# Performance work log

Hardware: AMD Instinct MI355X
Metric: run time of the kernel (lower is better)

The kernel has to match this reference:

```python
import jax, jax.numpy as jnp
import numpy as np

N_NODES = 100000


def gcn_conv(x, edge_index, W, b):
    """PyG GCNConv: h = x @ W; out = D^-1/2 (A+I) D^-1/2 h + b."""
    n = x.shape[0]
    src, dst = edge_index[0], edge_index[1]
    loop = jnp.arange(n)
    src = jnp.concatenate([src, loop])  # add self-loops
    dst = jnp.concatenate([dst, loop])
    # degree at target nodes (unit edge weights)
    deg = jax.ops.segment_sum(jnp.ones(dst.shape[0], dtype=x.dtype), dst, num_segments=n)
    dinv = jnp.where(deg > 0, jax.lax.rsqrt(deg), 0.0)
    norm = dinv[src] * dinv[dst]  # [E+n]
    h = x @ W  # [n, out]
    msg = h[src] * norm[:, None]  # gather + scale
    out = jax.ops.segment_sum(msg, dst, num_segments=n)  # scatter-add
    return out + b


def setup_inputs() -> dict:
    key = jax.random.key(0)
    k1, k2, k3, k4, k5, k6 = jax.random.split(key, 6)
    E = 3200000
    x = jax.random.normal(k1, (N_NODES, 2), dtype=jnp.float32)
    edge_index = jax.random.randint(k2, (2, E), 0, N_NODES, dtype=jnp.int64)
    W1 = jax.random.normal(k3, (2, 16), dtype=jnp.float32) * 0.5
    b1 = jax.random.normal(k4, (16,), dtype=jnp.float32) * 0.1
    W2 = jax.random.normal(k5, (16, 2), dtype=jnp.float32) * 0.25
    b2 = jax.random.normal(k6, (2,), dtype=jnp.float32) * 0.1
    return {"x": x, "edge_index": edge_index, "W1": W1, "b1": b1, "W2": W2, "b2": b2}


def reference(x, edge_index, W1, b1, W2, b2):
    h = jax.nn.relu(gcn_conv(x, edge_index, W1, b1))
    # dropout is identity at inference
    out = gcn_conv(h, edge_index, W2, b2)
    return jax.nn.log_softmax(out, axis=1)
```

## Files before the change

kernel.cpp:

```cpp
#include <hip/hip_runtime.h>
#include <math.h>


constexpr int N = 100000;
constexpr int LOGB = 6;
constexpr int BNODES = 1 << LOGB;
constexpr int K = (N + BNODES - 1) / BNODES;
constexpr int CAP = 2560;
constexpr int BS1 = 1024;
constexpr int EPT = 32;
constexpr int EPB = BS1 * EPT;

__global__ __launch_bounds__(1024) void k_partition(
    const int* __restrict__ src, const int* __restrict__ dst, int E,
    int* __restrict__ gfill, int* __restrict__ slots) {
    __shared__ int cnt[K];
    __shared__ int base[K];
    int t = threadIdx.x;
    for (int i = t; i < K; i += BS1) cnt[i] = 0;
    __syncthreads();
    int e0 = blockIdx.x * EPB;
    int e1 = min(E, e0 + EPB);
    for (int e = e0 + t; e < e1; e += BS1)
        atomicAdd(&cnt[dst[e] >> LOGB], 1);
    __syncthreads();
    for (int i = t; i < K; i += BS1) {
        int c = cnt[i];
        base[i] = (c > 0) ? atomicAdd(&gfill[i], c) : 0;
        cnt[i] = 0;
    }
    __syncthreads();
    for (int e = e0 + t; e < e1; e += BS1) {
        int d = dst[e];
        int s = src[e];
        int bin = d >> LOGB;
        int r = atomicAdd(&cnt[bin], 1);
        int pos = base[bin] + r;
        if (pos < CAP) slots[bin * CAP + pos] = (s << LOGB) | (d & (BNODES - 1));
    }
}

__global__ void k_degree(const int* __restrict__ gfill, const int* __restrict__ slots,
                         const float* __restrict__ x,
                         float* __restrict__ dinv, float2* __restrict__ sx) {
    __shared__ int cnt[BNODES];
    int b = blockIdx.x, t = threadIdx.x;
    if (t < BNODES) cnt[t] = 0;
    __syncthreads();
    int count = min(gfill[b], CAP);
    const int* row = slots + b * CAP;
    for (int j = t; j < count; j += blockDim.x)
        atomicAdd(&cnt[row[j] & (BNODES - 1)], 1);
    __syncthreads();
    if (t < BNODES) {
        int node = b * BNODES + t;
        if (node < N) {
            float di = rsqrtf((float)(cnt[t] + 1));
            dinv[node] = di;
            float2 xv = ((const float2*)x)[node];
            sx[node] = make_float2(xv.x * di, xv.y * di);
        }
    }
}

__global__ void k_agg1(const int* __restrict__ gfill, const int* __restrict__ slots,
                       const float* __restrict__ dinv, const float2* __restrict__ sx,
                       const float* __restrict__ W1, const float* __restrict__ b1,
                       const float* __restrict__ W2, float2* __restrict__ sz) {
    __shared__ float acc[BNODES * 2];
    __shared__ float sW1[32], sb1[16], sW2[32];
    int t = threadIdx.x;
    if (t < 32) sW1[t] = W1[t];
    if (t >= 32 && t < 48) sb1[t - 32] = b1[t - 32];
    if (t >= 48 && t < 80) sW2[t - 48] = W2[t - 48];
    if (t < BNODES * 2) acc[t] = 0.f;
    __syncthreads();
    int b = blockIdx.x;
    int count = min(gfill[b], CAP);
    const int* row = slots + b * CAP;
    for (int j = t; j < count; j += blockDim.x) {
        int p = row[j];
        float2 v = sx[p >> LOGB];
        int dl = p & (BNODES - 1);
        atomicAdd(&acc[2 * dl + 0], v.x);
        atomicAdd(&acc[2 * dl + 1], v.y);
    }
    __syncthreads();
    if (t < BNODES) {
        int node = b * BNODES + t;
        if (node < N) {
            float di = dinv[node];
            float2 sv = sx[node];
            float a0 = (acc[2 * t + 0] + sv.x) * di;
            float a1 = (acc[2 * t + 1] + sv.y) * di;
            float z0 = 0.f, z1 = 0.f;
#pragma unroll
            for (int k = 0; k < 16; k++) {
                float h = fmaf(a0, sW1[k], fmaf(a1, sW1[16 + k], sb1[k]));
                h = fmaxf(h, 0.f);
                z0 = fmaf(h, sW2[2 * k + 0], z0);
                z1 = fmaf(h, sW2[2 * k + 1], z1);
            }
            sz[node] = make_float2(z0 * di, z1 * di);
        }
    }
}

__global__ void k_agg2(const int* __restrict__ gfill, const int* __restrict__ slots,
                       const float* __restrict__ dinv, const float2* __restrict__ sz,
                       const float* __restrict__ b2, float2* __restrict__ out) {
    __shared__ float acc[BNODES * 2];
    int b = blockIdx.x, t = threadIdx.x;
    if (t < BNODES * 2) acc[t] = 0.f;
    __syncthreads();
    int count = min(gfill[b], CAP);
    const int* row = slots + b * CAP;
    for (int j = t; j < count; j += blockDim.x) {
        int p = row[j];
        float2 v = sz[p >> LOGB];
        int dl = p & (BNODES - 1);
        atomicAdd(&acc[2 * dl + 0], v.x);
        atomicAdd(&acc[2 * dl + 1], v.y);
    }
    __syncthreads();
    if (t < BNODES) {
        int node = b * BNODES + t;
        if (node < N) {
            float di = dinv[node];
            float2 sv = sz[node];
            float v0 = fmaf(acc[2 * t + 0] + sv.x, di, b2[0]);
            float v1 = fmaf(acc[2 * t + 1] + sv.y, di, b2[1]);
            float m = fmaxf(v0, v1);
            float lse = m + logf(expf(v0 - m) + expf(v1 - m));
            out[node] = make_float2(v0 - lse, v1 - lse);
        }
    }
}

extern "C" void kernel_launch(void* const* d_in, const int* in_sizes, int n_in,
                              void* d_out, int out_size, void* d_ws, size_t ws_size,
                              hipStream_t stream) {
    const float* x  = (const float*)d_in[0];
    const int*   ei = (const int*)d_in[1];
    const float* W1 = (const float*)d_in[2];
    const float* b1 = (const float*)d_in[3];
    const float* W2 = (const float*)d_in[4];
    const float* b2 = (const float*)d_in[5];

    const int E = in_sizes[1] / 2;
    const int* src = ei;
    const int* dst = ei + E;

    char* ws = (char*)d_ws;
    size_t off = 0;
    auto alloc = [&](size_t bytes) {
        char* p = ws + off;
        off += (bytes + 511) & ~size_t(511);
        return p;
    };
    int*    gfill = (int*)alloc(K * sizeof(int));
    float*  dinv  = (float*)alloc(N * sizeof(float));
    float2* sx    = (float2*)alloc(N * sizeof(float2));
    float2* sz    = (float2*)alloc(N * sizeof(float2));
    int*    slots = (int*)alloc((size_t)K * CAP * sizeof(int));

    hipMemsetAsync(gfill, 0, K * sizeof(int), stream);

    const int nblk1 = (E + EPB - 1) / EPB;
    k_partition<<<nblk1, BS1, 0, stream>>>(src, dst, E, gfill, slots);
    k_degree<<<K, 256, 0, stream>>>(gfill, slots, x, dinv, sx);
    k_agg1<<<K, 256, 0, stream>>>(gfill, slots, dinv, sx, W1, b1, W2, sz);
    k_agg2<<<K, 256, 0, stream>>>(gfill, slots, dinv, sz, b2, (float2*)d_out);
}
```

Baseline: 219.0 us.

## Replace atomic edge partition with count/scan/write passes and vectorize edge loads

Measured after the change: 552.0 us. 2.52x slower.

```diff
diff --git a/kernel.cpp b/kernel.cpp
--- a/kernel.cpp
+++ b/kernel.cpp
@@ -7,50 +7,95 @@
 constexpr int BNODES = 1 << LOGB;
 constexpr int K = (N + BNODES - 1) / BNODES;
 constexpr int CAP = 2560;
-constexpr int BS1 = 1024;
-constexpr int EPT = 32;
-constexpr int EPB = BS1 * EPT;
-
-__global__ __launch_bounds__(1024) void k_partition(
-    const int* __restrict__ src, const int* __restrict__ dst, int E,
-    int* __restrict__ gfill, int* __restrict__ slots) {
+constexpr int BSP = 256;
+constexpr int EPB = 4096;
+
+__global__ __launch_bounds__(BSP) void k_count(const int* __restrict__ dst, int E, int GP,
+                                               int* __restrict__ cntmat) {
     __shared__ int cnt[K];
-    __shared__ int base[K];
     int t = threadIdx.x;
-    for (int i = t; i < K; i += BS1) cnt[i] = 0;
+    for (int i = t; i < K; i += BSP) cnt[i] = 0;
     __syncthreads();
     int e0 = blockIdx.x * EPB;
     int e1 = min(E, e0 + EPB);
-    for (int e = e0 + t; e < e1; e += BS1)
-        atomicAdd(&cnt[dst[e] >> LOGB], 1);
-    __syncthreads();
-    for (int i = t; i < K; i += BS1) {
-        int c = cnt[i];
-        base[i] = (c > 0) ? atomicAdd(&gfill[i], c) : 0;
-        cnt[i] = 0;
-    }
-    __syncthreads();
-    for (int e = e0 + t; e < e1; e += BS1) {
-        int d = dst[e];
-        int s = src[e];
-        int bin = d >> LOGB;
-        int r = atomicAdd(&cnt[bin], 1);
-        int pos = base[bin] + r;
-        if (pos < CAP) slots[bin * CAP + pos] = (s << LOGB) | (d & (BNODES - 1));
-    }
-}
-
-__global__ void k_degree(const int* __restrict__ gfill, const int* __restrict__ slots,
-                         const float* __restrict__ x,
-                         float* __restrict__ dinv, float2* __restrict__ sx) {
+    int nvec = (e1 - e0) & ~3;
+    for (int e = e0 + 4 * t; e < e0 + nvec; e += 4 * BSP) {
+        int4 d4 = *(const int4*)(dst + e);
+        atomicAdd(&cnt[d4.x >> LOGB], 1);
+        atomicAdd(&cnt[d4.y >> LOGB], 1);
+        atomicAdd(&cnt[d4.z >> LOGB], 1);
+        atomicAdd(&cnt[d4.w >> LOGB], 1);
+    }
+    for (int e = e0 + nvec + t; e < e1; e += BSP) atomicAdd(&cnt[dst[e] >> LOGB], 1);
+    __syncthreads();
+    for (int i = t; i < K; i += BSP) cntmat[i * GP + blockIdx.x] = cnt[i];
+}
+
+__global__ void k_scan(int* __restrict__ cntmat, int GP, int* __restrict__ gfill) {
+    int bin = blockIdx.x * blockDim.x + threadIdx.x;
+    if (bin >= K) return;
+    int* row = cntmat + (size_t)bin * GP;
+    int sum = 0;
+    for (int b = 0; b < GP; b++) {
+        int c = row[b];
+        row[b] = sum;
+        sum += c;
+    }
+    gfill[bin] = sum;
+}
+
+__global__ __launch_bounds__(BSP) void k_write(const int* __restrict__ src,
+                                               const int* __restrict__ dst, int E, int GP,
+                                               const int* __restrict__ cntmat,
+                                               int* __restrict__ slots) {
+    __shared__ int cur[K];
+    int t = threadIdx.x;
+    for (int i = t; i < K; i += BSP) cur[i] = cntmat[i * GP + blockIdx.x];
+    __syncthreads();
+    int e0 = blockIdx.x * EPB;
+    int e1 = min(E, e0 + EPB);
+    int nvec = (e1 - e0) & ~3;
+    for (int e = e0 + 4 * t; e < e0 + nvec; e += 4 * BSP) {
+        int4 d4 = *(const int4*)(dst + e);
+        int4 s4 = *(const int4*)(src + e);
+        int b, r;
+        b = d4.x >> LOGB; r = atomicAdd(&cur[b], 1);
+        if (r < CAP) slots[b * CAP + r] = (s4.x << LOGB) | (d4.x & (BNODES - 1));
+        b = d4.y >> LOGB; r = atomicAdd(&cur[b], 1);
+        if (r < CAP) slots[b * CAP + r] = (s4.y << LOGB) | (d4.y & (BNODES - 1));
+        b = d4.z >> LOGB; r = atomicAdd(&cur[b], 1);
+        if (r < CAP) slots[b * CAP + r] = (s4.z << LOGB) | (d4.z & (BNODES - 1));
+        b = d4.w >> LOGB; r = atomicAdd(&cur[b], 1);
+        if (r < CAP) slots[b * CAP + r] = (s4.w << LOGB) | (d4.w & (BNODES - 1));
+    }
+    for (int e = e0 + nvec + t; e < e1; e += BSP) {
+        int d = dst[e], s = src[e];
+        int b = d >> LOGB;
+        int r = atomicAdd(&cur[b], 1);
+        if (r < CAP) slots[b * CAP + r] = (s << LOGB) | (d & (BNODES - 1));
+    }
+}
+
+__global__ __launch_bounds__(512) void k_degree(const int* __restrict__ gfill,
+                                                const int* __restrict__ slots,
+                                                const float* __restrict__ x,
+                                                float* __restrict__ dinv,
+                                                float2* __restrict__ sx) {
     __shared__ int cnt[BNODES];
     int b = blockIdx.x, t = threadIdx.x;
     if (t < BNODES) cnt[t] = 0;
     __syncthreads();
     int count = min(gfill[b], CAP);
     const int* row = slots + b * CAP;
-    for (int j = t; j < count; j += blockDim.x)
-        atomicAdd(&cnt[row[j] & (BNODES - 1)], 1);
+    int nvec = count & ~3;
+    for (int j = 4 * t; j < nvec; j += 4 * 512) {
+        int4 p = *(const int4*)(row + j);
+        atomicAdd(&cnt[p.x & (BNODES - 1)], 1);
+        atomicAdd(&cnt[p.y & (BNODES - 1)], 1);
+        atomicAdd(&cnt[p.z & (BNODES - 1)], 1);
+        atomicAdd(&cnt[p.w & (BNODES - 1)], 1);
+    }
+    for (int j = nvec + t; j < count; j += 512) atomicAdd(&cnt[row[j] & (BNODES - 1)], 1);
     __syncthreads();
     if (t < BNODES) {
         int node = b * BNODES + t;
@@ -63,10 +108,14 @@
     }
 }
 
-__global__ void k_agg1(const int* __restrict__ gfill, const int* __restrict__ slots,
-                       const float* __restrict__ dinv, const float2* __restrict__ sx,
-                       const float* __restrict__ W1, const float* __restrict__ b1,
-                       const float* __restrict__ W2, float2* __restrict__ sz) {
+__global__ __launch_bounds__(512) void k_agg1(const int* __restrict__ gfill,
+                                              const int* __restrict__ slots,
+                                              const float* __restrict__ dinv,
+                                              const float2* __restrict__ sx,
+                                              const float* __restrict__ W1,
+                                              const float* __restrict__ b1,
+                                              const float* __restrict__ W2,
+                                              float2* __restrict__ sz) {
     __shared__ float acc[BNODES * 2];
     __shared__ float sW1[32], sb1[16], sW2[32];
     int t = threadIdx.x;
@@ -78,12 +127,25 @@
     int b = blockIdx.x;
     int count = min(gfill[b], CAP);
     const int* row = slots + b * CAP;
-    for (int j = t; j < count; j += blockDim.x) {
+    int nvec = count & ~3;
+    for (int j = 4 * t; j < nvec; j += 4 * 512) {
+        int4 p = *(const int4*)(row + j);
+        float2 v0 = sx[p.x >> LOGB], v1 = sx[p.y >> LOGB];
+        float2 v2 = sx[p.z >> LOGB], v3 = sx[p.w >> LOGB];
+        atomicAdd(&acc[2 * (p.x & (BNODES - 1)) + 0], v0.x);
+        atomicAdd(&acc[2 * (p.x & (BNODES - 1)) + 1], v0.y);
+        atomicAdd(&acc[2 * (p.y & (BNODES - 1)) + 0], v1.x);
+        atomicAdd(&acc[2 * (p.y & (BNODES - 1)) + 1], v1.y);
+        atomicAdd(&acc[2 * (p.z & (BNODES - 1)) + 0], v2.x);
+        atomicAdd(&acc[2 * (p.z & (BNODES - 1)) + 1], v2.y);
+        atomicAdd(&acc[2 * (p.w & (BNODES - 1)) + 0], v3.x);
+        atomicAdd(&acc[2 * (p.w & (BNODES - 1)) + 1], v3.y);
+    }
+    for (int j = nvec + t; j < count; j += 512) {
         int p = row[j];
         float2 v = sx[p >> LOGB];
-        int dl = p & (BNODES - 1);
-        atomicAdd(&acc[2 * dl + 0], v.x);
-        atomicAdd(&acc[2 * dl + 1], v.y);
+        atomicAdd(&acc[2 * (p & (BNODES - 1)) + 0], v.x);
+        atomicAdd(&acc[2 * (p & (BNODES - 1)) + 1], v.y);
     }
     __syncthreads();
     if (t < BNODES) {
@@ -106,21 +168,37 @@
     }
 }
 
-__global__ void k_agg2(const int* __restrict__ gfill, const int* __restrict__ slots,
-                       const float* __restrict__ dinv, const float2* __restrict__ sz,
-                       const float* __restrict__ b2, float2* __restrict__ out) {
+__global__ __launch_bounds__(512) void k_agg2(const int* __restrict__ gfill,
+                                              const int* __restrict__ slots,
+                                              const float* __restrict__ dinv,
+                                              const float2* __restrict__ sz,
+                                              const float* __restrict__ b2,
+                                              float2* __restrict__ out) {
     __shared__ float acc[BNODES * 2];
     int b = blockIdx.x, t = threadIdx.x;
     if (t < BNODES * 2) acc[t] = 0.f;
     __syncthreads();
     int count = min(gfill[b], CAP);
     const int* row = slots + b * CAP;
-    for (int j = t; j < count; j += blockDim.x) {
+    int nvec = count & ~3;
+    for (int j = 4 * t; j < nvec; j += 4 * 512) {
+        int4 p = *(const int4*)(row + j);
+        float2 v0 = sz[p.x >> LOGB], v1 = sz[p.y >> LOGB];
+        float2 v2 = sz[p.z >> LOGB], v3 = sz[p.w >> LOGB];
+        atomicAdd(&acc[2 * (p.x & (BNODES - 1)) + 0], v0.x);
+        atomicAdd(&acc[2 * (p.x & (BNODES - 1)) + 1], v0.y);
+        atomicAdd(&acc[2 * (p.y & (BNODES - 1)) + 0], v1.x);
+        atomicAdd(&acc[2 * (p.y & (BNODES - 1)) + 1], v1.y);
+        atomicAdd(&acc[2 * (p.z & (BNODES - 1)) + 0], v2.x);
+        atomicAdd(&acc[2 * (p.z & (BNODES - 1)) + 1], v2.y);
+        atomicAdd(&acc[2 * (p.w & (BNODES - 1)) + 0], v3.x);
+        atomicAdd(&acc[2 * (p.w & (BNODES - 1)) + 1], v3.y);
+    }
+    for (int j = nvec + t; j < count; j += 512) {
         int p = row[j];
         float2 v = sz[p >> LOGB];
-        int dl = p & (BNODES - 1);
-        atomicAdd(&acc[2 * dl + 0], v.x);
-        atomicAdd(&acc[2 * dl + 1], v.y);
+        atomicAdd(&acc[2 * (p & (BNODES - 1)) + 0], v.x);
+        atomicAdd(&acc[2 * (p & (BNODES - 1)) + 1], v.y);
     }
     __syncthreads();
     if (t < BNODES) {
@@ -150,6 +228,7 @@
     const int E = in_sizes[1] / 2;
     const int* src = ei;
     const int* dst = ei + E;
+    const int GP = (E + EPB - 1) / EPB;
 
     char* ws = (char*)d_ws;
     size_t off = 0;
@@ -158,17 +237,17 @@
         off += (bytes + 511) & ~size_t(511);
         return p;
     };
-    int*    gfill = (int*)alloc(K * sizeof(int));
-    float*  dinv  = (float*)alloc(N * sizeof(float));
-    float2* sx    = (float2*)alloc(N * sizeof(float2));
-    float2* sz    = (float2*)alloc(N * sizeof(float2));
-    int*    slots = (int*)alloc((size_t)K * CAP * sizeof(int));
-
-    hipMemsetAsync(gfill, 0, K * sizeof(int), stream);
-
-    const int nblk1 = (E + EPB - 1) / EPB;
-    k_partition<<<nblk1, BS1, 0, stream>>>(src, dst, E, gfill, slots);
-    k_degree<<<K, 256, 0, stream>>>(gfill, slots, x, dinv, sx);
-    k_agg1<<<K, 256, 0, stream>>>(gfill, slots, dinv, sx, W1, b1, W2, sz);
-    k_agg2<<<K, 256, 0, stream>>>(gfill, slots, dinv, sz, b2, (float2*)d_out);
-}
+    int*    gfill  = (int*)alloc(K * sizeof(int));
+    float*  dinv   = (float*)alloc(N * sizeof(float));
+    float2* sx     = (float2*)alloc(N * sizeof(float2));
+    float2* sz     = (float2*)alloc(N * sizeof(float2));
+    int*    cntmat = (int*)alloc((size_t)K * GP * sizeof(int));
+    int*    slots  = (int*)alloc((size_t)K * CAP * sizeof(int));
+
+    k_count<<<GP, BSP, 0, stream>>>(dst, E, GP, cntmat);
+    k_scan<<<(K + 255) / 256, 256, 0, stream>>>(cntmat, GP, gfill);
+    k_write<<<GP, BSP, 0, stream>>>(src, dst, E, GP, cntmat, slots);
+    k_degree<<<K, 512, 0, stream>>>(gfill, slots, x, dinv, sx);
+    k_agg1<<<K, 512, 0, stream>>>(gfill, slots, dinv, sx, W1, b1, W2, sz);
+    k_agg2<<<K, 512, 0, stream>>>(gfill, slots, dinv, sz, b2, (float2*)d_out);
+}
```
